# Optimization experiments

Measured on AMD Instinct MI355X. Metric: run time of the kernel, lower is better.

Reference implementation:

```python
import jax, jax.numpy as jnp
import numpy as np

N_NODES = 1_000_000
N_EDGES = 16_000_000
D = 30            # num_feature hardcoded in the module
WINDOW = D // 6   # = 5
DEG_THRESH = 10
NUM_TYPES = 2


def setup_inputs() -> dict:
    key = jax.random.key(0)
    k1, k2, k3, k4 = jax.random.split(key, 4)
    x = jax.random.normal(k1, (N_NODES, D), dtype=jnp.float32)
    W = jax.random.normal(k2, (D, D), dtype=jnp.float32)
    edge_index = jax.random.randint(k3, (2, N_EDGES), 0, N_NODES, dtype=jnp.int64)
    atom_types = jax.random.randint(k4, (N_NODES,), 0, NUM_TYPES, dtype=jnp.int64)
    return {"x": x, "W": W, "edge_index": edge_index, "atom_types": atom_types}


def reference(x, W, edge_index, atom_types):
    n = x.shape[0]
    # --- degree count: torch.bincount(edge_index.reshape(-1)) ---
    flat = edge_index.reshape(-1)
    count = jnp.zeros((n,), jnp.int32).at[flat].add(1)
    crit_count = (count > DEG_THRESH).astype(jnp.int32)  # criterion_count

    # --- type-mixture scatter-min over edges ---
    src, dst = edge_index[0], edge_index[1]
    same = atom_types[src] == atom_types[dst]
    # edge contributes 0 if types differ, else type+1, to BOTH endpoints; take min
    val = jnp.where(same, atom_types[src].astype(jnp.int32) + 1, 0)
    BIG = jnp.iinfo(jnp.int32).max
    mix = jnp.full((n,), BIG, jnp.int32)
    mix = mix.at[src].min(val).at[dst].min(val)
    mix = jnp.where(mix == BIG, 0, mix)  # isolated atoms -> 0

    crit = crit_count * 3 + mix  # criterion in [0, 5]

    # --- windowed one-hot criterion matrix [n, D] ---
    cols = jnp.arange(D, dtype=jnp.int32)
    start = (crit * WINDOW)[:, None]
    mask = ((cols[None, :] >= start) & (cols[None, :] < start + WINDOW)).astype(x.dtype)

    # --- e3nn Linear (30x0e -> 30x0e): dense matmul with 1/sqrt(fan_in) path norm ---
    scale = np.float32(1.0 / np.sqrt(D))
    return (x @ W) * scale * mask
```

## Files before the change

### kernel.cpp

```cpp
#include <hip/hip_runtime.h>

#define N_NODES    1000000
#define N_EDGES    16000000
#define D          30
#define WINDOW     5
#define DEG_THRESH 10

#define P_PARTS    31
#define PART_BITS  15
#define PART_SIZE  32768
#define CAP        1081344
#define BUF_CAP    512
#define BIN_BLOCKS 256
#define BIN_THREADS 1024
#define BIN_ITERS  16
#define N_GROUPS   (N_EDGES / 4)
#define BM_WORDS   (N_NODES / 32)

#define L_BM_BYTES   125000
#define L_BUF_BYTES  (P_PARTS * BUF_CAP * 2)
#define L_CNT_OFF    (L_BM_BYTES + L_BUF_BYTES)
#define L_TOTAL      (L_CNT_OFF + P_PARTS * 4 * 3)

#define SLICES     8
#define HIST_WORDS 16384

#define WS_BM_OFF      0
#define WS_CUR_OFF     131072
#define WS_PART_OFF    131328
#define WS_NEEDED      (WS_PART_OFF + (size_t)P_PARTS * SLICES * HIST_WORDS * 4)
#define OUT_BYTES_NEEDED ((size_t)P_PARTS * CAP * 2)

__global__ __launch_bounds__(256) void pack_types(
    const int* __restrict__ types,
    unsigned*  __restrict__ bm,
    unsigned*  __restrict__ cursors)
{
    const int g = blockIdx.x * 256 + threadIdx.x;
    const int v = (g < N_NODES) ? types[g] : 0;
    const unsigned long long m = __ballot(v);
    if ((threadIdx.x & 31) == 0 && g < N_NODES)
        bm[g >> 5] = (unsigned)(m >> (threadIdx.x & 32));
    if (blockIdx.x == 0 && threadIdx.x < 64) cursors[threadIdx.x] = 0u;
}

__global__ __launch_bounds__(BIN_THREADS, 1) void bin_edges(
    const int*      __restrict__ edge_index,
    const unsigned* __restrict__ bm,
    unsigned short* __restrict__ buckets,
    unsigned*       __restrict__ cursors)
{
    extern __shared__ char smem[];
    unsigned* bm_lds = (unsigned*)smem;
    unsigned short (*buf)[BUF_CAP] =
        (unsigned short(*)[BUF_CAP])(smem + L_BM_BYTES);
    unsigned* cnt   = (unsigned*)(smem + L_CNT_OFF);
    unsigned* basev = cnt + P_PARTS;
    unsigned* ccnt  = basev + P_PARTS;

    const int tid = threadIdx.x;
    for (int i = tid; i < BM_WORDS; i += BIN_THREADS) bm_lds[i] = bm[i];
    if (tid < P_PARTS) cnt[tid] = 0u;
    __syncthreads();

    for (int it = 0; it < BIN_ITERS; ++it) {
        const int g = (blockIdx.x * BIN_ITERS + it) * BIN_THREADS + tid;
        if (g < N_GROUPS) {
            const int e0 = g * 4;
            const int4 s4 = *reinterpret_cast<const int4*>(edge_index + e0);
            const int4 d4 = *reinterpret_cast<const int4*>(edge_index + N_EDGES + e0);
            const int ss[4] = {s4.x, s4.y, s4.z, s4.w};
            const int dd[4] = {d4.x, d4.y, d4.z, d4.w};
#pragma unroll
            for (int k = 0; k < 4; ++k) {
                const int s = ss[k], d = dd[k];
                const unsigned ts = (bm_lds[(unsigned)s >> 5] >> (s & 31)) & 1u;
                const unsigned td = (bm_lds[(unsigned)d >> 5] >> (d & 31)) & 1u;
                {
                    const int b = s >> PART_BITS;
                    const unsigned short rec =
                        (unsigned short)(((s & (PART_SIZE - 1)) << 1) | td);
                    const unsigned pos = atomicAdd(&cnt[b], 1u);
                    if (pos < BUF_CAP) buf[b][pos] = rec;
                    else {
                        const unsigned gp = atomicAdd(&cursors[b], 1u);
                        if (gp < CAP) buckets[(size_t)b * CAP + gp] = rec;
                    }
                }
                {
                    const int b = d >> PART_BITS;
                    const unsigned short rec =
                        (unsigned short)(((d & (PART_SIZE - 1)) << 1) | ts);
                    const unsigned pos = atomicAdd(&cnt[b], 1u);
                    if (pos < BUF_CAP) buf[b][pos] = rec;
                    else {
                        const unsigned gp = atomicAdd(&cursors[b], 1u);
                        if (gp < CAP) buckets[(size_t)b * CAP + gp] = rec;
                    }
                }
            }
        }
        __syncthreads();
        if (tid < P_PARTS) {
            unsigned c = cnt[tid]; if (c > BUF_CAP) c = BUF_CAP;
            unsigned bse = 0u;
            if (c) {
                bse = atomicAdd(&cursors[tid], c);
                if (bse > CAP) bse = CAP;
                if (bse + c > CAP) c = CAP - bse;
            }
            ccnt[tid] = c; basev[tid] = bse; cnt[tid] = 0u;
        }
        __syncthreads();
        const int w = tid >> 6, lane = tid & 63;
#pragma unroll
        for (int j = 0; j < 2; ++j) {
            const int b = w * 2 + j;
            if (b < P_PARTS) {
                const unsigned c = ccnt[b];
                unsigned short* dst = buckets + (size_t)b * CAP + basev[b];
                for (unsigned e = lane; e < c; e += 64) dst[e] = buf[b][e];
            }
        }
        __syncthreads();
    }
}

__global__ __launch_bounds__(512) void hist_pass(
    const unsigned short* __restrict__ buckets,
    const unsigned*       __restrict__ cursors,
    unsigned*             __restrict__ partials)
{
    __shared__ unsigned hist[HIST_WORDS];
    const int p = blockIdx.x >> 3, s = blockIdx.x & 7;
    const int tid = threadIdx.x;
    for (int i = tid; i < HIST_WORDS; i += 512) hist[i] = 0u;
    __syncthreads();

    unsigned count = cursors[p]; if (count > CAP) count = CAP;
    const unsigned short* bk = buckets + (size_t)p * CAP;
    const unsigned n4 = (count + 3u) >> 2;
    for (unsigned j = (unsigned)(s * 512 + tid); j < n4; j += SLICES * 512) {
        const unsigned i0 = j * 4u;
        if (i0 + 4u <= count) {
            const ushort4 r4 = *reinterpret_cast<const ushort4*>(bk + i0);
            const unsigned short rr[4] = {r4.x, r4.y, r4.z, r4.w};
#pragma unroll
            for (int k = 0; k < 4; ++k) {
                const unsigned rec = rr[k];
                const unsigned local = rec >> 1, t = rec & 1u;
                atomicAdd(&hist[local >> 1], (1u << (8u * t)) << (16u * (local & 1u)));
            }
        } else {
            for (unsigned i = i0; i < count; ++i) {
                const unsigned rec = bk[i];
                const unsigned local = rec >> 1, t = rec & 1u;
                atomicAdd(&hist[local >> 1], (1u << (8u * t)) << (16u * (local & 1u)));
            }
        }
    }
    __syncthreads();
    unsigned* op = partials + (size_t)blockIdx.x * HIST_WORDS;
    for (int i = tid; i < HIST_WORDS; i += 512) op[i] = hist[i];
}

#define ONPB 256
__global__ __launch_bounds__(256) void out_pass(
    const float* __restrict__ x, const float* __restrict__ Wm,
    const unsigned* __restrict__ partials,
    const unsigned* __restrict__ bm,
    float* __restrict__ out)
{
    __shared__ float sx[ONPB * 31];
    __shared__ float sW[D * D];
    __shared__ unsigned char sst[ONPB];
    const int tid   = threadIdx.x;
    const long base = (long)blockIdx.x * ONPB;
    const long tot  = (long)N_NODES * D;

    for (int i = tid; i < D * D; i += 256) sW[i] = Wm[i];
    for (int i = tid; i < ONPB * D; i += 256) {
        const int n = i / D, c = i - n * D;
        const long gi = base * D + i;
        sx[n * 31 + c] = (gi < tot) ? x[gi] : 0.0f;
    }
    if (tid < ONPB / 2) {
        const unsigned Wd = (unsigned)(base >> 1) + tid;
        unsigned st0 = 0, st1 = 0;
        if (Wd < N_NODES / 2) {
            const unsigned p = Wd >> 14, widx = Wd & 16383u;
            const unsigned* pp = partials + (size_t)(p * SLICES) * HIST_WORDS + widx;
            unsigned sum = 0u;
#pragma unroll
            for (int s = 0; s < SLICES; ++s) sum += pp[(size_t)s * HIST_WORDS];
            const unsigned bmw = bm[Wd >> 4];
            unsigned st[2];
#pragma unroll
            for (int h = 0; h < 2; ++h) {
                const unsigned c0 = (sum >> (16 * h)) & 0xFFu;
                const unsigned c1 = (sum >> (16 * h + 8)) & 0xFFu;
                const unsigned t  = (bmw >> ((Wd & 15u) * 2u + (unsigned)h)) & 1u;
                const unsigned cnt    = c0 + c1;
                const unsigned same_c = t ? c1 : c0;
                const unsigned diff_c = t ? c0 : c1;
                const int mix  = diff_c ? 0 : (same_c ? (int)t + 1 : 0);
                const int crit = (cnt > DEG_THRESH ? 3 : 0) + mix;
                st[h] = (unsigned)(crit * WINDOW);
            }
            st0 = st[0]; st1 = st[1];
        }
        sst[2 * tid]     = (unsigned char)st0;
        sst[2 * tid + 1] = (unsigned char)st1;
    }
    __syncthreads();

    float xr[D];
#pragma unroll
    for (int k = 0; k < D; ++k) xr[k] = sx[tid * 31 + k];
    const int start = sst[tid];
    float acc[WINDOW];
#pragma unroll
    for (int cc = 0; cc < WINDOW; ++cc) {
        const int col = start + cc;
        float a = 0.0f;
#pragma unroll
        for (int k = 0; k < D; ++k) a += xr[k] * sW[k * D + col];
        acc[cc] = a * 0.18257418583505536f;
    }
    __syncthreads();
#pragma unroll
    for (int k = 0; k < D; ++k) sx[tid * 31 + k] = 0.0f;
#pragma unroll
    for (int cc = 0; cc < WINDOW; ++cc) sx[tid * 31 + start + cc] = acc[cc];
    __syncthreads();
    for (int i = tid; i < ONPB * D; i += 256) {
        const int n = i / D, c = i - n * D;
        const long gi = base * D + i;
        if (gi < tot) out[gi] = sx[n * 31 + c];
    }
}

#define SAME_INC (1u << 12)
#define DIFF_INC (1u << 22)

__global__ __launch_bounds__(256) void edge_pass_atomic(
    const int* __restrict__ edge_index, const int* __restrict__ atom_types,
    unsigned* __restrict__ agg)
{
    const int t  = blockIdx.x * blockDim.x + threadIdx.x;
    const int e0 = t * 4;
    if (e0 >= N_EDGES) return;
    const int4 s4 = *reinterpret_cast<const int4*>(edge_index + e0);
    const int4 d4 = *reinterpret_cast<const int4*>(edge_index + N_EDGES + e0);
    const int ss[4] = {s4.x, s4.y, s4.z, s4.w};
    const int dd[4] = {d4.x, d4.y, d4.z, d4.w};
#pragma unroll
    for (int k = 0; k < 4; ++k) {
        const int s = ss[k], d = dd[k];
        const unsigned add = 1u + ((atom_types[s] == atom_types[d]) ? SAME_INC : DIFF_INC);
        atomicAdd(agg + s, add);
        atomicAdd(agg + d, add);
    }
}

__global__ __launch_bounds__(256) void out_pass_agg(
    const float* __restrict__ x, const float* __restrict__ Wm,
    const unsigned* __restrict__ agg, const int* __restrict__ atom_types,
    float* __restrict__ out)
{
    __shared__ float sx[64 * D];
    __shared__ float sW[D * D];
    __shared__ int   sstart[64];
    const int tid   = threadIdx.x;
    const long base = (long)blockIdx.x * 64;
    for (int i = tid; i < D * D; i += 256) sW[i] = Wm[i];
    const float* xb = x + base * D;
    for (int i = tid; i < 64 * D; i += 256) sx[i] = xb[i];
    if (tid < 64) {
        const long n = base + tid;
        const unsigned a = agg[n];
        const int cnt = a & 0xFFFu, sc = (a >> 12) & 0x3FFu, dc = a >> 22;
        const int mix  = dc ? 0 : (sc ? atom_types[n] + 1 : 0);
        sstart[tid] = ((cnt > DEG_THRESH ? 3 : 0) + mix) * WINDOW;
    }
    __syncthreads();
    const float scale = 0.18257418583505536f;
    float* ob = out + base * D;
    for (int i = tid; i < 64 * D; i += 256) {
        const int nd = i / D, c = i - nd * D;
        float v = 0.0f;
        if ((unsigned)(c - sstart[nd]) < WINDOW) {
            float acc = 0.0f;
#pragma unroll
            for (int k = 0; k < D; ++k) acc += sx[nd * D + k] * sW[k * D + c];
            v = acc * scale;
        }
        ob[i] = v;
    }
}

extern "C" void kernel_launch(void* const* d_in, const int* in_sizes, int n_in,
                              void* d_out, int out_size, void* d_ws, size_t ws_size,
                              hipStream_t stream)
{
    const float* x          = (const float*)d_in[0];
    const float* Wm         = (const float*)d_in[1];
    const int*   edge_index = (const int*)d_in[2];
    const int*   atom_types = (const int*)d_in[3];
    float* out = (float*)d_out;

    if (ws_size >= WS_NEEDED && (size_t)out_size * 4 >= OUT_BYTES_NEEDED) {
        char* ws = (char*)d_ws;
        unsigned*       bm       = (unsigned*)(ws + WS_BM_OFF);
        unsigned*       cursors  = (unsigned*)(ws + WS_CUR_OFF);
        unsigned*       partials = (unsigned*)(ws + WS_PART_OFF);
        unsigned short* buckets  = (unsigned short*)d_out;

        pack_types<<<(N_NODES + 255) / 256, 256, 0, stream>>>(atom_types, bm, cursors);
        bin_edges<<<BIN_BLOCKS, BIN_THREADS, L_TOTAL, stream>>>(edge_index, bm,
                                                                buckets, cursors);
        hist_pass<<<P_PARTS * SLICES, 512, 0, stream>>>(buckets, cursors, partials);
        out_pass<<<(N_NODES + ONPB - 1) / ONPB, 256, 0, stream>>>(
            x, Wm, partials, bm, out);
    } else {
        unsigned* agg = (unsigned*)d_ws;
        hipMemsetAsync(agg, 0x00, N_NODES * sizeof(unsigned), stream);
        edge_pass_atomic<<<(N_EDGES / 4) / 256, 256, 0, stream>>>(edge_index, atom_types, agg);
        out_pass_agg<<<N_NODES / 64, 256, 0, stream>>>(x, Wm, agg, atom_types, out);
    }
}
```

Baseline: 422.2 us.

## Rewrite out_pass to load and store rows directly per thread without LDS staging

The output kernel no longer stages x tiles and output tiles through shared memory with several barriers. Each thread now reads its node's 30 floats as float2 directly from global memory, computes its criterion itself, and writes the full masked row as float2 stores. W is kept transposed in LDS with padding so each window column is read contiguously. This drops the LDS round trips and syncs, but the per-thread strided global accesses coalesce less well than the old cooperative block-wide copies.

```diff
diff --git a/kernel.cpp b/kernel.cpp
--- a/kernel.cpp
+++ b/kernel.cpp
@@ -164,80 +164,74 @@
     for (int i = tid; i < HIST_WORDS; i += 512) op[i] = hist[i];
 }
 
-#define ONPB 256
-__global__ __launch_bounds__(256) void out_pass(
+#define WT_STRIDE 36
+__global__ __launch_bounds__(512) void out_pass(
     const float* __restrict__ x, const float* __restrict__ Wm,
     const unsigned* __restrict__ partials,
     const unsigned* __restrict__ bm,
     float* __restrict__ out)
 {
-    __shared__ float sx[ONPB * 31];
-    __shared__ float sW[D * D];
-    __shared__ unsigned char sst[ONPB];
-    const int tid   = threadIdx.x;
-    const long base = (long)blockIdx.x * ONPB;
-    const long tot  = (long)N_NODES * D;
-
-    for (int i = tid; i < D * D; i += 256) sW[i] = Wm[i];
-    for (int i = tid; i < ONPB * D; i += 256) {
-        const int n = i / D, c = i - n * D;
-        const long gi = base * D + i;
-        sx[n * 31 + c] = (gi < tot) ? x[gi] : 0.0f;
-    }
-    if (tid < ONPB / 2) {
-        const unsigned Wd = (unsigned)(base >> 1) + tid;
-        unsigned st0 = 0, st1 = 0;
-        if (Wd < N_NODES / 2) {
-            const unsigned p = Wd >> 14, widx = Wd & 16383u;
-            const unsigned* pp = partials + (size_t)(p * SLICES) * HIST_WORDS + widx;
-            unsigned sum = 0u;
-#pragma unroll
-            for (int s = 0; s < SLICES; ++s) sum += pp[(size_t)s * HIST_WORDS];
-            const unsigned bmw = bm[Wd >> 4];
-            unsigned st[2];
-#pragma unroll
-            for (int h = 0; h < 2; ++h) {
-                const unsigned c0 = (sum >> (16 * h)) & 0xFFu;
-                const unsigned c1 = (sum >> (16 * h + 8)) & 0xFFu;
-                const unsigned t  = (bmw >> ((Wd & 15u) * 2u + (unsigned)h)) & 1u;
-                const unsigned cnt    = c0 + c1;
-                const unsigned same_c = t ? c1 : c0;
-                const unsigned diff_c = t ? c0 : c1;
-                const int mix  = diff_c ? 0 : (same_c ? (int)t + 1 : 0);
-                const int crit = (cnt > DEG_THRESH ? 3 : 0) + mix;
-                st[h] = (unsigned)(crit * WINDOW);
-            }
-            st0 = st[0]; st1 = st[1];
-        }
-        sst[2 * tid]     = (unsigned char)st0;
-        sst[2 * tid + 1] = (unsigned char)st1;
-    }
-    __syncthreads();
+    __shared__ float sWt[D * WT_STRIDE];
+    const int tid = threadIdx.x;
+    for (int i = tid; i < D * D; i += 512) {
+        const int k = i / D, c = i - k * D;
+        sWt[c * WT_STRIDE + k] = Wm[i];
+    }
+    __syncthreads();
+
+    const long n = (long)blockIdx.x * 512 + tid;
+    if (n >= N_NODES) return;
+
+    const unsigned Wd   = (unsigned)(n >> 1);
+    const unsigned h    = (unsigned)n & 1u;
+    const unsigned p    = Wd >> 14;
+    const unsigned widx = Wd & 16383u;
+    const unsigned* pp  = partials + (size_t)(p * SLICES) * HIST_WORDS + widx;
+    unsigned sum = 0u;
+#pragma unroll
+    for (int s = 0; s < SLICES; ++s) sum += pp[(size_t)s * HIST_WORDS];
+    const unsigned c0 = (sum >> (16u * h)) & 0xFFu;
+    const unsigned c1 = (sum >> (16u * h + 8u)) & 0xFFu;
+    const unsigned t  = (bm[n >> 5] >> ((unsigned)n & 31u)) & 1u;
+    const unsigned cnt    = c0 + c1;
+    const unsigned same_c = t ? c1 : c0;
+    const unsigned diff_c = t ? c0 : c1;
+    const int mix  = diff_c ? 0 : (same_c ? (int)t + 1 : 0);
+    const int crit = (cnt > DEG_THRESH ? 3 : 0) + mix;
 
     float xr[D];
-#pragma unroll
-    for (int k = 0; k < D; ++k) xr[k] = sx[tid * 31 + k];
-    const int start = sst[tid];
+    const float2* xb = reinterpret_cast<const float2*>(x + (size_t)n * D);
+#pragma unroll
+    for (int i = 0; i < D / 2; ++i) {
+        const float2 v = xb[i];
+        xr[2 * i] = v.x; xr[2 * i + 1] = v.y;
+    }
+
     float acc[WINDOW];
-#pragma unroll
-    for (int cc = 0; cc < WINDOW; ++cc) {
-        const int col = start + cc;
+    const float* wc0 = &sWt[(crit * WINDOW) * WT_STRIDE];
+#pragma unroll
+    for (int j = 0; j < WINDOW; ++j) {
+        const float* wc = wc0 + j * WT_STRIDE;
         float a = 0.0f;
 #pragma unroll
-        for (int k = 0; k < D; ++k) a += xr[k] * sW[k * D + col];
-        acc[cc] = a * 0.18257418583505536f;
-    }
-    __syncthreads();
-#pragma unroll
-    for (int k = 0; k < D; ++k) sx[tid * 31 + k] = 0.0f;
-#pragma unroll
-    for (int cc = 0; cc < WINDOW; ++cc) sx[tid * 31 + start + cc] = acc[cc];
-    __syncthreads();
-    for (int i = tid; i < ONPB * D; i += 256) {
-        const int n = i / D, c = i - n * D;
-        const long gi = base * D + i;
-        if (gi < tot) out[gi] = sx[n * 31 + c];
-    }
+        for (int k = 0; k < D; ++k) a += xr[k] * wc[k];
+        acc[j] = a * 0.18257418583505536f;
+    }
+
+    float2 o[D / 2];
+#pragma unroll
+    for (int q = 0; q < D / WINDOW; ++q) {
+        const bool m = (q == crit);
+#pragma unroll
+        for (int r = 0; r < WINDOW; ++r) {
+            const float v = m ? acc[r] : 0.0f;
+            const int c = WINDOW * q + r;
+            if (c & 1) o[c >> 1].y = v; else o[c >> 1].x = v;
+        }
+    }
+    float2* ob = reinterpret_cast<float2*>(out + (size_t)n * D);
+#pragma unroll
+    for (int i = 0; i < D / 2; ++i) ob[i] = o[i];
 }
 
 #define SAME_INC (1u << 12)
@@ -320,7 +314,7 @@
         bin_edges<<<BIN_BLOCKS, BIN_THREADS, L_TOTAL, stream>>>(edge_index, bm,
                                                                 buckets, cursors);
         hist_pass<<<P_PARTS * SLICES, 512, 0, stream>>>(buckets, cursors, partials);
-        out_pass<<<(N_NODES + ONPB - 1) / ONPB, 256, 0, stream>>>(
+        out_pass<<<(N_NODES + 511) / 512, 512, 0, stream>>>(
             x, Wm, partials, bm, out);
     } else {
         unsigned* agg = (unsigned*)d_ws;
```

After: 395.6 us. -6.3%, faster.
